# Optimization experiments

Hardware: AMD Instinct MI355X
Metric: run time of the kernel (lower is better)

## Reference

```python
import jax, jax.numpy as jnp
import numpy as np

HEAD_SIZE = 64
N_EMB = 384
B, S = 512, 256

def setup_inputs() -> dict:
    key = jax.random.key(0)
    k1, k2, k3, k4 = jax.random.split(key, 4)
    x = jax.random.normal(k1, (B, S, N_EMB), dtype=jnp.float32)
    scale = 1.0 / np.sqrt(N_EMB)
    Wq = jax.random.normal(k2, (N_EMB, HEAD_SIZE), dtype=jnp.float32) * scale
    Wk = jax.random.normal(k3, (N_EMB, HEAD_SIZE), dtype=jnp.float32) * scale
    Wv = jax.random.normal(k4, (N_EMB, HEAD_SIZE), dtype=jnp.float32) * scale
    return {"x": x, "Wq": Wq, "Wk": Wk, "Wv": Wv}

def reference(x, Wq, Wk, Wv):
    # Projections (Linear, no bias): [B,S,E] @ [E,H] -> [B,S,H]
    q = jnp.einsum('bse,eh->bsh', x, Wq)
    k = jnp.einsum('bse,eh->bsh', x, Wk)
    v = jnp.einsum('bse,eh->bsh', x, Wv)
    # Scores: [B,S,S], scaled by 1/sqrt(head_size)
    scores = jnp.einsum('bqh,bkh->bqk', q, k) / jnp.sqrt(jnp.asarray(HEAD_SIZE, x.dtype))
    seq_len = x.shape[1]
    causal = jnp.tril(jnp.ones((seq_len, seq_len), dtype=bool))
    scores = jnp.where(causal[None, :, :], scores, jnp.asarray(-jnp.inf, scores.dtype))
    attn = jax.nn.softmax(scores, axis=-1)
    # dropout_ratio=0 -> identity
    out = jnp.einsum('bqk,bkh->bqh', attn, v)
    return out
```

## Files before the change

kernel.cpp:

```cpp
#include <hip/hip_runtime.h>
#include <hip/hip_bf16.h>


#define NB   512
#define SS   256
#define EE   384
#define HH   64

#define PR16  16
#define LROW  392
#define XLSZ  (PR16 * LROW)

#define SYNC_LDS() asm volatile("s_waitcnt lgkmcnt(0)\n\ts_barrier" ::: "memory")

typedef short bf16x8 __attribute__((ext_vector_type(8)));
typedef float f32x4  __attribute__((ext_vector_type(4)));

__device__ __forceinline__ short f2bf(float f) {
  union { float f; unsigned u; } x; x.f = f;
  unsigned r = x.u + 0x7fffu + ((x.u >> 16) & 1u);
  return (short)(r >> 16);
}

__global__ __launch_bounds__(256) void prep_w_kernel(
    const float* __restrict__ Wq, const float* __restrict__ Wk,
    const float* __restrict__ Wv, short* __restrict__ wfrag) {
  int t = blockIdx.x * 256 + threadIdx.x;
  if (t >= 12 * 12 * 64) return;
  int ks  = t / (12 * 64);
  int rem = t % (12 * 64);
  int nf  = rem / 64;
  int l   = rem % 64;
  int l15 = l & 15, lhi = l >> 4;
  int ncat = nf * 16 + l15;
  const float* W = (ncat < 64) ? Wq : (ncat < 128 ? Wk : Wv);
  int n = ncat & 63;
  short* dst = wfrag + (size_t)t * 8;
#pragma unroll
  for (int j = 0; j < 8; ++j) {
    int kk = ks * 32 + lhi * 8 + j;
    dst[j] = f2bf(W[kk * 64 + n]);
  }
}

__global__ __launch_bounds__(512, 2) void fused_kernel(
    const float* __restrict__ x, const short* __restrict__ wfrag,
    float* __restrict__ out) {
  __shared__ __align__(16) short Ql[SS * HH];
  __shared__ __align__(16) short Kl[SS * HH];
  __shared__ __align__(16) short Vt[HH * SS];
  __shared__ __align__(16) short xst[4 * XLSZ];

  int b    = blockIdx.x;
  int tid  = threadIdx.x;
  int lane = tid & 63, wv = tid >> 6;
  int l15  = lane & 15, lhi = lane >> 4;
  int sw   = l15 & 7;
  int g    = wv >> 2;
  int wg   = wv & 3;
  int tg   = tid & 255;
  const float* xg = x + (size_t)b * SS * EE + (size_t)g * 128 * EE;

  bf16x8 af[12][3];
#pragma unroll
  for (int ks = 0; ks < 12; ++ks)
#pragma unroll
    for (int ht = 0; ht < 3; ++ht)
      af[ks][ht] = *(const bf16x8*)(wfrag + ((size_t)(ks * 12 + wg * 3 + ht) * 64 + lane) * 8);
#pragma unroll
  for (int ks = 0; ks < 12; ++ks)
#pragma unroll
    for (int ht = 0; ht < 3; ++ht)
      asm volatile("" : "+v"(af[ks][ht]));

  f32x4 st[6];
  auto loadch = [&](int ch) {
    const float* p0 = xg + (size_t)ch * PR16 * EE;
#pragma unroll
    for (int i = 0; i < 3; ++i) {
      const f32x4* p = (const f32x4*)(p0 + (size_t)(tg + 256 * i) * 8);
      st[2 * i]     = p[0];
      st[2 * i + 1] = p[1];
    }
  };
  auto writech = [&](short* xl) {
#pragma unroll
    for (int i = 0; i < 3; ++i) {
      int c = tg + 256 * i;
      int row = c / 48, cg = c % 48;
      union { bf16x8 vv; __hip_bfloat162 h2[4]; } u;
      u.h2[0] = __float22bfloat162_rn(make_float2(st[2*i][0],   st[2*i][1]));
      u.h2[1] = __float22bfloat162_rn(make_float2(st[2*i][2],   st[2*i][3]));
      u.h2[2] = __float22bfloat162_rn(make_float2(st[2*i+1][0], st[2*i+1][1]));
      u.h2[3] = __float22bfloat162_rn(make_float2(st[2*i+1][2], st[2*i+1][3]));
      *(bf16x8*)(xl + row * LROW + cg * 8) = u.vv;
    }
  };

  loadch(0);
  writech(xst + (g * 2) * XLSZ);
  for (int ch = 0; ch < 8; ++ch) {
    if (ch < 7) loadch(ch + 1);
    SYNC_LDS();
    const short* xl = xst + (g * 2 + (ch & 1)) * XLSZ;

    f32x4 acc[3];
#pragma unroll
    for (int ht = 0; ht < 3; ++ht) acc[ht] = (f32x4){0.f, 0.f, 0.f, 0.f};
#pragma unroll
    for (int ks = 0; ks < 12; ++ks) {
      bf16x8 bx = *(const bf16x8*)(xl + l15 * LROW + ks * 32 + lhi * 8);
#pragma unroll
      for (int ht = 0; ht < 3; ++ht)
        acc[ht] = __builtin_amdgcn_mfma_f32_16x16x32_bf16(af[ks][ht], bx, acc[ht], 0, 0, 0);
    }

    int row  = g * 128 + ch * PR16 + l15;
    int srow = ((row & 8) >> 1) | (row & 3);
#pragma unroll
    for (int ht = 0; ht < 3; ++ht) {
      int f = wg * 3 + ht;
      int ncat = f * 16 + lhi * 4;
      if (f < 4) {
        union { short4 s4; __hip_bfloat162 h2[2]; } oq;
        oq.h2[0] = __float22bfloat162_rn(make_float2(acc[ht][0], acc[ht][1]));
        oq.h2[1] = __float22bfloat162_rn(make_float2(acc[ht][2], acc[ht][3]));
        *(short4*)(Ql + row * 64 + (ncat ^ ((row & 7) << 3))) = oq.s4;
      } else if (f < 8) {
        int col = ncat - 64;
        union { short4 s4; __hip_bfloat162 h2[2]; } ok;
        ok.h2[0] = __float22bfloat162_rn(make_float2(acc[ht][0], acc[ht][1]));
        ok.h2[1] = __float22bfloat162_rn(make_float2(acc[ht][2], acc[ht][3]));
        *(short4*)(Kl + row * 64 + (col ^ (srow << 3))) = ok.s4;
      } else {
#pragma unroll
        for (int j = 0; j < 4; ++j) {
          int h = ncat - 128 + j;
          Vt[h * 256 + (row ^ ((h & 7) << 3))] = f2bf(acc[ht][j]);
        }
      }
    }
    if (ch < 7) writech(xst + (g * 2 + ((ch + 1) & 1)) * XLSZ);
  }
  SYNC_LDS();

  size_t obase = (size_t)b * SS * HH;
#pragma unroll
  for (int u = 0; u < 2; ++u) {
    int rt    = (u == 0) ? wv : (15 - wv);
    int qrow0 = rt * 16;
    int twp   = (rt + 2) & ~1;
    int nk    = twp >> 1;
    int qg    = qrow0 + l15;

    int qlrow = qrow0 + l15;
    bf16x8 qa0 = *(const bf16x8*)(Ql + qlrow * 64 + ((lhi * 8) ^ ((qlrow & 7) << 3)));
    bf16x8 qa1 = *(const bf16x8*)(Ql + qlrow * 64 + ((32 + lhi * 8) ^ ((qlrow & 7) << 3)));

    f32x4 s[16];
#pragma unroll
    for (int t = 0; t < 16; ++t) {
      if (t >= twp) continue;
      int kc = (t >> 1) * 32 + ((l15 >> 2) << 3) + ((t & 1) << 2) + (l15 & 3);
      const short* kp = Kl + kc * 64;
      bf16x8 kb0 = *(const bf16x8*)(kp + ((lhi * 8) ^ (sw << 3)));
      bf16x8 kb1 = *(const bf16x8*)(kp + ((32 + lhi * 8) ^ (sw << 3)));
      __builtin_amdgcn_s_setprio(1);
      f32x4 a = (f32x4){0.f, 0.f, 0.f, 0.f};
      a = __builtin_amdgcn_mfma_f32_16x16x32_bf16(kb0, qa0, a, 0, 0, 0);
      a = __builtin_amdgcn_mfma_f32_16x16x32_bf16(kb1, qa1, a, 0, 0, 0);
      __builtin_amdgcn_s_setprio(0);
#pragma unroll
      for (int r = 0; r < 4; ++r) {
        int kg = (t >> 1) * 32 + lhi * 8 + ((t & 1) << 2) + r;
        s[t][r] = (kg <= qg) ? a[r] * 0.125f : -INFINITY;
      }
    }

    float mx = -3.0e38f;
#pragma unroll
    for (int t = 0; t < 16; ++t) {
      if (t >= twp) continue;
#pragma unroll
      for (int r = 0; r < 4; ++r) mx = fmaxf(mx, s[t][r]);
    }
    mx = fmaxf(mx, __shfl_xor(mx, 16));
    mx = fmaxf(mx, __shfl_xor(mx, 32));
    float sm = 0.f;
#pragma unroll
    for (int t = 0; t < 16; ++t) {
      if (t >= twp) continue;
#pragma unroll
      for (int r = 0; r < 4; ++r) {
        float p = __expf(s[t][r] - mx);
        s[t][r] = p;
        sm += p;
      }
    }
    sm += __shfl_xor(sm, 16);
    sm += __shfl_xor(sm, 32);
    float inv = 1.f / sm;
    float invq[4];
#pragma unroll
    for (int r = 0; r < 4; ++r) invq[r] = __shfl(inv, lhi * 4 + r);

    f32x4 o[4];
#pragma unroll
    for (int nf = 0; nf < 4; ++nf) o[nf] = (f32x4){0.f, 0.f, 0.f, 0.f};
#pragma unroll
    for (int kc2 = 0; kc2 < 8; ++kc2) {
      if (kc2 >= nk) continue;
      union { bf16x8 v; __hip_bfloat162 h2[4]; } pu;
      pu.h2[0] = __float22bfloat162_rn(make_float2(s[2*kc2][0],   s[2*kc2][1]));
      pu.h2[1] = __float22bfloat162_rn(make_float2(s[2*kc2][2],   s[2*kc2][3]));
      pu.h2[2] = __float22bfloat162_rn(make_float2(s[2*kc2+1][0], s[2*kc2+1][1]));
      pu.h2[3] = __float22bfloat162_rn(make_float2(s[2*kc2+1][2], s[2*kc2+1][3]));
      int kofs = kc2 * 32 + lhi * 8;
      __builtin_amdgcn_s_setprio(1);
#pragma unroll
      for (int nf = 0; nf < 4; ++nf) {
        int hrow = nf * 16 + l15;
        bf16x8 vb = *(const bf16x8*)(Vt + hrow * 256 + (kofs ^ ((hrow & 7) << 3)));
        o[nf] = __builtin_amdgcn_mfma_f32_16x16x32_bf16(pu.v, vb, o[nf], 0, 0, 0);
      }
      __builtin_amdgcn_s_setprio(0);
    }

#pragma unroll
    for (int nf = 0; nf < 4; ++nf)
#pragma unroll
      for (int r = 0; r < 4; ++r) {
        int q = qrow0 + lhi * 4 + r;
        int h = nf * 16 + l15;
        out[obase + (size_t)q * HH + h] = o[nf][r] * invq[r];
      }
  }
}

extern "C" void kernel_launch(void* const* d_in, const int* in_sizes, int n_in,
                              void* d_out, int out_size, void* d_ws, size_t ws_size,
                              hipStream_t stream) {
  const float* x  = (const float*)d_in[0];
  const float* Wq = (const float*)d_in[1];
  const float* Wk = (const float*)d_in[2];
  const float* Wv = (const float*)d_in[3];
  float* out = (float*)d_out;

  short* wfrag = (short*)d_ws;

  prep_w_kernel<<<36, 256, 0, stream>>>(Wq, Wk, Wv, wfrag);
  fused_kernel<<<512, 512, 0, stream>>>(x, wfrag, out);
}
```

Before: 56.99 us.

## Process two batches per block and prefetch the next batch during attention

Halves the grid to 256 blocks, so each block runs two batch elements in sequence. While the first batch's attention phase runs, it loads the next batch's first x chunk and issues touch loads over that batch's remaining rows to pull them into cache. The aim is to hide the global-load latency at the start of each projection phase and to overlap memory traffic with attention compute. The cost is extra registers for the prefetched chunk, reloading the weight fragments on every iteration, and fewer blocks for the scheduler to balance.

Result: slower. 125.7 us (+120.6%).

```diff
diff --git a/kernel.cpp b/kernel.cpp
--- a/kernel.cpp
+++ b/kernel.cpp
@@ -51,7 +51,7 @@
   __shared__ __align__(16) short Vt[HH * SS];
   __shared__ __align__(16) short xst[4 * XLSZ];
 
-  int b    = blockIdx.x;
+  int b0   = blockIdx.x;
   int tid  = threadIdx.x;
   int lane = tid & 63, wv = tid >> 6;
   int l15  = lane & 15, lhi = lane >> 4;
@@ -59,23 +59,10 @@
   int g    = wv >> 2;
   int wg   = wv & 3;
   int tg   = tid & 255;
-  const float* xg = x + (size_t)b * SS * EE + (size_t)g * 128 * EE;
-
-  bf16x8 af[12][3];
-#pragma unroll
-  for (int ks = 0; ks < 12; ++ks)
-#pragma unroll
-    for (int ht = 0; ht < 3; ++ht)
-      af[ks][ht] = *(const bf16x8*)(wfrag + ((size_t)(ks * 12 + wg * 3 + ht) * 64 + lane) * 8);
-#pragma unroll
-  for (int ks = 0; ks < 12; ++ks)
-#pragma unroll
-    for (int ht = 0; ht < 3; ++ht)
-      asm volatile("" : "+v"(af[ks][ht]));
 
   f32x4 st[6];
-  auto loadch = [&](int ch) {
-    const float* p0 = xg + (size_t)ch * PR16 * EE;
+  auto loadch = [&](const float* xgp, int ch) {
+    const float* p0 = xgp + (size_t)ch * PR16 * EE;
 #pragma unroll
     for (int i = 0; i < 3; ++i) {
       const f32x4* p = (const f32x4*)(p0 + (size_t)(tg + 256 * i) * 8);
@@ -97,57 +84,7 @@
     }
   };
 
-  loadch(0);
-  writech(xst + (g * 2) * XLSZ);
-  for (int ch = 0; ch < 8; ++ch) {
-    if (ch < 7) loadch(ch + 1);
-    SYNC_LDS();
-    const short* xl = xst + (g * 2 + (ch & 1)) * XLSZ;
-
-    f32x4 acc[3];
-#pragma unroll
-    for (int ht = 0; ht < 3; ++ht) acc[ht] = (f32x4){0.f, 0.f, 0.f, 0.f};
-#pragma unroll
-    for (int ks = 0; ks < 12; ++ks) {
-      bf16x8 bx = *(const bf16x8*)(xl + l15 * LROW + ks * 32 + lhi * 8);
-#pragma unroll
-      for (int ht = 0; ht < 3; ++ht)
-        acc[ht] = __builtin_amdgcn_mfma_f32_16x16x32_bf16(af[ks][ht], bx, acc[ht], 0, 0, 0);
-    }
-
-    int row  = g * 128 + ch * PR16 + l15;
-    int srow = ((row & 8) >> 1) | (row & 3);
-#pragma unroll
-    for (int ht = 0; ht < 3; ++ht) {
-      int f = wg * 3 + ht;
-      int ncat = f * 16 + lhi * 4;
-      if (f < 4) {
-        union { short4 s4; __hip_bfloat162 h2[2]; } oq;
-        oq.h2[0] = __float22bfloat162_rn(make_float2(acc[ht][0], acc[ht][1]));
-        oq.h2[1] = __float22bfloat162_rn(make_float2(acc[ht][2], acc[ht][3]));
-        *(short4*)(Ql + row * 64 + (ncat ^ ((row & 7) << 3))) = oq.s4;
-      } else if (f < 8) {
-        int col = ncat - 64;
-        union { short4 s4; __hip_bfloat162 h2[2]; } ok;
-        ok.h2[0] = __float22bfloat162_rn(make_float2(acc[ht][0], acc[ht][1]));
-        ok.h2[1] = __float22bfloat162_rn(make_float2(acc[ht][2], acc[ht][3]));
-        *(short4*)(Kl + row * 64 + (col ^ (srow << 3))) = ok.s4;
-      } else {
-#pragma unroll
-        for (int j = 0; j < 4; ++j) {
-          int h = ncat - 128 + j;
-          Vt[h * 256 + (row ^ ((h & 7) << 3))] = f2bf(acc[ht][j]);
-        }
-      }
-    }
-    if (ch < 7) writech(xst + (g * 2 + ((ch + 1) & 1)) * XLSZ);
-  }
-  SYNC_LDS();
-
-  size_t obase = (size_t)b * SS * HH;
-#pragma unroll
-  for (int u = 0; u < 2; ++u) {
-    int rt    = (u == 0) ? wv : (15 - wv);
+  auto attn_tile = [&](int rt, size_t obase) {
     int qrow0 = rt * 16;
     int twp   = (rt + 2) & ~1;
     int nk    = twp >> 1;
@@ -234,6 +171,91 @@
         int h = nf * 16 + l15;
         out[obase + (size_t)q * HH + h] = o[nf][r] * invq[r];
       }
+  };
+
+  {
+    const float* xg0 = x + (size_t)b0 * SS * EE + (size_t)g * 128 * EE;
+    loadch(xg0, 0);
+    writech(xst + (g * 2) * XLSZ);
+  }
+
+  for (int it = 0; it < 2; ++it) {
+    int b = b0 + it * 256;
+    const float* xg = x + (size_t)b * SS * EE + (size_t)g * 128 * EE;
+
+    bf16x8 af[12][3];
+#pragma unroll
+    for (int ks = 0; ks < 12; ++ks)
+#pragma unroll
+      for (int ht = 0; ht < 3; ++ht)
+        af[ks][ht] = *(const bf16x8*)(wfrag + ((size_t)(ks * 12 + wg * 3 + ht) * 64 + lane) * 8);
+#pragma unroll
+    for (int ks = 0; ks < 12; ++ks)
+#pragma unroll
+      for (int ht = 0; ht < 3; ++ht)
+        asm volatile("" : "+v"(af[ks][ht]));
+
+    for (int ch = 0; ch < 8; ++ch) {
+      if (ch < 7) loadch(xg, ch + 1);
+      SYNC_LDS();
+      const short* xl = xst + (g * 2 + (ch & 1)) * XLSZ;
+
+      f32x4 acc[3];
+#pragma unroll
+      for (int ht = 0; ht < 3; ++ht) acc[ht] = (f32x4){0.f, 0.f, 0.f, 0.f};
+#pragma unroll
+      for (int ks = 0; ks < 12; ++ks) {
+        bf16x8 bx = *(const bf16x8*)(xl + l15 * LROW + ks * 32 + lhi * 8);
+#pragma unroll
+        for (int ht = 0; ht < 3; ++ht)
+          acc[ht] = __builtin_amdgcn_mfma_f32_16x16x32_bf16(af[ks][ht], bx, acc[ht], 0, 0, 0);
+      }
+
+      int row  = g * 128 + ch * PR16 + l15;
+      int srow = ((row & 8) >> 1) | (row & 3);
+#pragma unroll
+      for (int ht = 0; ht < 3; ++ht) {
+        int f = wg * 3 + ht;
+        int ncat = f * 16 + lhi * 4;
+        if (f < 4) {
+          union { short4 s4; __hip_bfloat162 h2[2]; } oq;
+          oq.h2[0] = __float22bfloat162_rn(make_float2(acc[ht][0], acc[ht][1]));
+          oq.h2[1] = __float22bfloat162_rn(make_float2(acc[ht][2], acc[ht][3]));
+          *(short4*)(Ql + row * 64 + (ncat ^ ((row & 7) << 3))) = oq.s4;
+        } else if (f < 8) {
+          int col = ncat - 64;
+          union { short4 s4; __hip_bfloat162 h2[2]; } ok;
+          ok.h2[0] = __float22bfloat162_rn(make_float2(acc[ht][0], acc[ht][1]));
+          ok.h2[1] = __float22bfloat162_rn(make_float2(acc[ht][2], acc[ht][3]));
+          *(short4*)(Kl + row * 64 + (col ^ (srow << 3))) = ok.s4;
+        } else {
+#pragma unroll
+          for (int j = 0; j < 4; ++j) {
+            int h = ncat - 128 + j;
+            Vt[h * 256 + (row ^ ((h & 7) << 3))] = f2bf(acc[ht][j]);
+          }
+        }
+      }
+      if (ch < 7) writech(xst + (g * 2 + ((ch + 1) & 1)) * XLSZ);
+    }
+    SYNC_LDS();
+
+    size_t obase = (size_t)b * SS * HH;
+    if (it == 0) {
+      const float* xgn = x + (size_t)(b0 + 256) * SS * EE + (size_t)g * 128 * EE;
+      loadch(xgn, 0);
+      float dummy = 0.f;
+      const float* px = xgn + 16 * EE;
+#pragma unroll
+      for (int i = 0; i < 6; ++i) {
+        int c = tg + i * 256;
+        if (c < 1344) dummy += px[(size_t)c * 32];
+      }
+      asm volatile("" :: "v"(dummy));
+    }
+    attn_tile(wv, obase);
+    if (it == 0) writech(xst + (g * 2) * XLSZ);
+    attn_tile(15 - wv, obase);
   }
 }
 
@@ -249,5 +271,5 @@
   short* wfrag = (short*)d_ws;
 
   prep_w_kernel<<<36, 256, 0, stream>>>(Wq, Wk, Wv, wfrag);
-  fused_kernel<<<512, 512, 0, stream>>>(x, wfrag, out);
-}
+  fused_kernel<<<256, 512, 0, stream>>>(x, wfrag, out);
+}
```
